# Kernel tuning notes

Measured on AMD Instinct MI355X. Metric: run time of the kernel, lower is better.

Reference implementation:

```python
import jax, jax.numpy as jnp
import numpy as np

STRIDES = (8, 16, 32, 64, 128)
NUM_CONVS = 4
GROUPS = 32
EPS = 1e-5
FEAT_SHAPES = [(8, 256, 100, 152), (8, 256, 50, 76), (8, 256, 25, 38), (8, 256, 13, 19), (8, 256, 7, 10)]


def _conv3x3(x, w, b):
    # x: [B,C,H,W], w: [O,I,3,3] -> SAME padding, stride 1
    y = jax.lax.conv_general_dilated(x, w, (1, 1), 'SAME', dimension_numbers=('NCHW', 'OIHW', 'NCHW'))
    return y + b[None, :, None, None]


def _group_norm(x, g, b):
    B, C, H, W = x.shape
    xr = x.reshape(B, GROUPS, C // GROUPS, H, W)
    m = xr.mean(axis=(2, 3, 4), keepdims=True)
    v = xr.var(axis=(2, 3, 4), keepdims=True)
    xr = (xr - m) * jax.lax.rsqrt(v + EPS)
    return xr.reshape(B, C, H, W) * g[None, :, None, None] + b[None, :, None, None]


def _head(feats, cls_w, cls_b, cls_gn_g, cls_gn_b, box_w, box_b, box_gn_g, box_gn_b,
          logits_w, logits_b, ctr_w, ctr_b, reg_w, reg_b, scales):
    outs = []
    for l, f in enumerate(feats):
        ct, bt = f, f
        for i in range(NUM_CONVS):  # fixed-depth tower loop
            ct = jax.nn.relu(_group_norm(_conv3x3(ct, cls_w[i], cls_b[i]), cls_gn_g[i], cls_gn_b[i]))
            bt = jax.nn.relu(_group_norm(_conv3x3(bt, box_w[i], box_b[i]), box_gn_g[i], box_gn_b[i]))
        logits = _conv3x3(ct, logits_w, logits_b)          # [B,80,H,W]
        ctr = _conv3x3(ct, ctr_w, ctr_b)                   # [B,1,H,W]
        reg = jnp.exp(scales[l] * _conv3x3(bt, reg_w, reg_b))  # [B,4,H,W], torch.exp(Scale(bbox_pred))
        B = f.shape[0]
        outs.append(jnp.concatenate([logits, reg, ctr], axis=1).reshape(B, -1))
    return jnp.concatenate(outs, axis=1)  # [B, sum_l 85*H_l*W_l]


def _locations(feats):
    # FCOS grid locations: (x,y) center of each stride cell, per level, concatenated
    locs = []
    for l, f in enumerate(feats):
        h, w = f.shape[-2:]
        s = STRIDES[l]
        sx = jnp.arange(w, dtype=jnp.float32) * s + s // 2
        sy = jnp.arange(h, dtype=jnp.float32) * s + s // 2
        yy, xx = jnp.meshgrid(sy, sx, indexing='ij')
        locs.append(jnp.stack([xx.reshape(-1), yy.reshape(-1)], axis=1))
    return jnp.concatenate(locs, axis=0)  # [sum HW, 2]


def setup_inputs() -> dict:
    key = jax.random.key(0)
    ks = jax.random.split(key, 12)
    d = {}
    for i, s in enumerate(FEAT_SHAPES):
        d['feat%d' % i] = jax.random.normal(ks[i], s, dtype=jnp.float32)

    def w(k, shape):
        return jax.random.normal(k, shape, dtype=jnp.float32) * 0.01  # init std=0.01

    d['cls_w'] = w(ks[5], (NUM_CONVS, 256, 256, 3, 3))
    d['cls_b'] = jnp.zeros((NUM_CONVS, 256), jnp.float32)
    d['cls_gn_g'] = jnp.ones((NUM_CONVS, 256), jnp.float32)
    d['cls_gn_b'] = jnp.zeros((NUM_CONVS, 256), jnp.float32)
    d['box_w'] = w(ks[6], (NUM_CONVS, 256, 256, 3, 3))
    d['box_b'] = jnp.zeros((NUM_CONVS, 256), jnp.float32)
    d['box_gn_g'] = jnp.ones((NUM_CONVS, 256), jnp.float32)
    d['box_gn_b'] = jnp.zeros((NUM_CONVS, 256), jnp.float32)
    d['logits_w'] = w(ks[7], (80, 256, 3, 3))
    d['logits_b'] = jnp.full((80,), -float(np.log((1.0 - 0.01) / 0.01)), jnp.float32)  # prior_prob bias
    d['ctr_w'] = w(ks[8], (1, 256, 3, 3))
    d['ctr_b'] = jnp.zeros((1,), jnp.float32)
    d['reg_w'] = w(ks[9], (4, 256, 3, 3))
    d['reg_b'] = jnp.zeros((4,), jnp.float32)
    d['scales'] = jnp.ones((5,), jnp.float32)
    return d


def reference(feat0, feat1, feat2, feat3, feat4, cls_w, cls_b, cls_gn_g, cls_gn_b,
              box_w, box_b, box_gn_g, box_gn_b, logits_w, logits_b, ctr_w, ctr_b,
              reg_w, reg_b, scales):
    feats = [feat0, feat1, feat2, feat3, feat4]
    out = _head(feats, cls_w, cls_b, cls_gn_g, cls_gn_b, box_w, box_b, box_gn_g, box_gn_b,
                logits_w, logits_b, ctr_w, ctr_b, reg_w, reg_b, scales)
    locs = _locations(feats)
    return out, locs
```

## Files before the change

### kernel.cpp

```cpp
#include <hip/hip_runtime.h>
#include <hip/hip_bf16.h>

#define TOT85 1722695ULL

using short8 = __attribute__((ext_vector_type(8))) short;
using f32x4  = __attribute__((ext_vector_type(4))) float;

struct Feat5 { const float* p[5]; };

__device__ __forceinline__ float bfbits2f(short u) {
  return __uint_as_float(((unsigned int)(unsigned short)u) << 16);
}
__device__ __forceinline__ short f2bfbits(float f) {
  __hip_bfloat16 h = __float2bfloat16(f);
  return *reinterpret_cast<short*>(&h);
}

#define LVL_TABLES                                                              \
  constexpr int kH[5] = {100, 50, 25, 13, 7};                                   \
  constexpr int kW[5] = {152, 76, 38, 19, 10};                                  \
  constexpr int kNTx[5] = {10, 5, 3, 2, 1};                                     \
  constexpr int kCumT[5] = {0, 130, 165, 177, 181};                             \
  constexpr int kCumHW[5] = {0, 15200, 19000, 19950, 20197};                    \
  constexpr float kInv[5] = {1.f / 121600.f, 1.f / 30400.f, 1.f / 7600.f,       \
                             1.f / 1976.f, 1.f / 560.f};

__global__ __launch_bounds__(256) void repack_k(const float* __restrict__ src,
                                                __hip_bfloat16* __restrict__ dst,
                                                int O, int NOCP, int ocoff) {
  int idx = blockIdx.x * 256 + threadIdx.x;
  if (idx >= O * 2304) return;
  int o = idx / 2304;
  int r = idx - o * 2304;
  int i = r / 9;
  int t = r - i * 9;
  dst[((size_t)(t * 8 + (i >> 5)) * NOCP + (o + ocoff)) * 32 + (i & 31)] =
      __float2bfloat16(src[idx]);
}

__global__ void locations_all_k(float* __restrict__ out) {
  LVL_TABLES
  constexpr int kStride[5] = {8, 16, 32, 64, 128};
  int i = blockIdx.x * 256 + threadIdx.x;
  if (i >= 20267) return;
  int lvl = (i >= 15200) + (i >= 19000) + (i >= 19950) + (i >= 20197);
  int local = i - kCumHW[lvl];
  int W = kW[lvl];
  float s = (float)kStride[lvl];
  int y = local / W, x = local - y * W;
  out[2 * i + 0] = x * s + 0.5f * s;
  out[2 * i + 1] = y * s + 0.5f * s;
}

template <bool NORM_IN, bool SRC_NCHW>
__global__ __launch_bounds__(256, 2) void conv_tower_k(
    Feat5 feats, const __hip_bfloat16* __restrict__ srcb_base,
    const __hip_bfloat16* __restrict__ wpk, const float* __restrict__ bias,
    const float* __restrict__ statsInBase, const float* __restrict__ gamma,
    const float* __restrict__ beta, __hip_bfloat16* __restrict__ dstBase,
    float* __restrict__ statsOutBase) {
  LVL_TABLES
  __shared__ __align__(16) short s_in[180 * 72];
  __shared__ float s_red[64];
  __shared__ float s_a[256], s_c[256];

  const int tid = threadIdx.x;
  const int lane = tid & 63;
  const int wave = tid >> 6;
  const int wm = wave >> 1;
  const int wn = wave & 1;
  const int bx = blockIdx.x;
  const int lvl = (bx >= 130) + (bx >= 165) + (bx >= 177) + (bx >= 181);
  const int H = kH[lvl], W = kW[lvl], nTx = kNTx[lvl];
  const int tloc = bx - kCumT[lvl];
  const int ty = tloc / nTx, tx = tloc - ty * nTx;
  const int x0 = tx * 16, y0 = ty * 8;
  const int b = blockIdx.z;
  const int HW = H * W;
  const size_t lbase = (size_t)2048 * kCumHW[lvl];
  const int l15 = lane & 15;
  const int kg = lane >> 4;
  const int q8x = (tid & 7) * 8;

  if (tid < 64) s_red[tid] = 0.f;
  if (NORM_IN) {
    const float* statsIn = statsInBase + (size_t)lvl * 4096;
    float inv_cnt = kInv[lvl];
    int g = tid >> 3;
    float s = statsIn[(b * 32 + g) * 2 + 0];
    float ss = statsIn[(b * 32 + g) * 2 + 1];
    float m = s * inv_cnt;
    float var = fmaf(-m, m, ss * inv_cnt);
    float rs = rsqrtf(var + 1e-5f);
    float avv = rs * gamma[tid];
    s_a[tid] = avv;
    s_c[tid] = fmaf(-m, avv, beta[tid]);
  }

  f32x4 acc[4][8];
#pragma unroll
  for (int m = 0; m < 4; ++m)
#pragma unroll
    for (int n = 0; n < 8; ++n) acc[m][n] = (f32x4){0.f, 0.f, 0.f, 0.f};

  const short* wlane = (const short*)wpk + ((wn * 128 + l15) * 32 + kg * 8);

  const int pixN = tid;
  int prowN = pixN / 18;
  int pcolN = pixN - prowN * 18;
  const int gyN = y0 + prowN - 1, gxN = x0 + pcolN - 1;
  const bool validN = (pixN < 180) && (gyN >= 0 && gyN < H && gxN >= 0 && gxN < W);

  for (int c = 0; c < 4; ++c) {
    const int ic0 = c * 64;

    short8 pv[6];
    float fv[32];
    if (SRC_NCHW) {
      const float* srcf = feats.p[lvl];
      if (validN) {
        const float* p = srcf + (((size_t)(b * 256 + ic0)) * H + gyN) * W + gxN;
#pragma unroll
        for (int j = 0; j < 32; ++j) fv[j] = p[(size_t)j * HW];
      }
    } else {
      const short* srcb = (const short*)srcb_base + lbase;
#pragma unroll
      for (int r = 0; r < 6; ++r) {
        int idx = r * 256 + tid;
        pv[r] = (short8)0;
        if (idx < 1440) {
          int px = idx >> 3;
          int prow = px / 18;
          int pcol = px - prow * 18;
          int gy = y0 + prow - 1, gx = x0 + pcol - 1;
          if (gy >= 0 && gy < H && gx >= 0 && gx < W)
            pv[r] = *(const short8*)(srcb +
                                     ((((size_t)b * H + gy) * W + gx) * 256 + ic0 + q8x));
        }
      }
    }

    __syncthreads();

    if (SRC_NCHW) {
      const float* srcf = feats.p[lvl];
      if (pixN < 180) {
        short8 sv[4];
        if (validN) {
#pragma unroll
          for (int q = 0; q < 4; ++q)
#pragma unroll
            for (int j = 0; j < 8; ++j) sv[q][j] = f2bfbits(fv[q * 8 + j]);
        } else {
#pragma unroll
          for (int q = 0; q < 4; ++q) sv[q] = (short8)0;
        }
#pragma unroll
        for (int q = 0; q < 4; ++q) *(short8*)(s_in + pixN * 72 + q * 8) = sv[q];
        if (validN) {
          const float* p = srcf + (((size_t)(b * 256 + ic0 + 32)) * H + gyN) * W + gxN;
#pragma unroll
          for (int j = 0; j < 32; ++j) fv[j] = p[(size_t)j * HW];
#pragma unroll
          for (int q = 0; q < 4; ++q)
#pragma unroll
            for (int j = 0; j < 8; ++j) sv[q][j] = f2bfbits(fv[q * 8 + j]);
        }
#pragma unroll
        for (int q = 0; q < 4; ++q) *(short8*)(s_in + pixN * 72 + 32 + q * 8) = sv[q];
      }
    } else {
      float av[8], cv[8];
#pragma unroll
      for (int j = 0; j < 8; ++j) {
        int c2 = ic0 + q8x + j;
        av[j] = s_a[c2];
        cv[j] = s_c[c2];
      }
#pragma unroll
      for (int r = 0; r < 6; ++r) {
        int idx = r * 256 + tid;
        if (idx < 1440) {
          int px = idx >> 3;
          int prow = px / 18;
          int pcol = px - prow * 18;
          int gy = y0 + prow - 1, gx = x0 + pcol - 1;
          short8 o8 = (short8)0;
          if (gy >= 0 && gy < H && gx >= 0 && gx < W) {
#pragma unroll
            for (int j = 0; j < 8; ++j)
              o8[j] = f2bfbits(fmaxf(fmaf(bfbits2f(pv[r][j]), av[j], cv[j]), 0.f));
          }
          *(short8*)(s_in + px * 72 + q8x) = o8;
        }
      }
    }
    __syncthreads();

    const short* wcb = wlane + (size_t)c * 2 * 8192;
    short8 bwA[8], bwB[8];
#pragma unroll
    for (int n = 0; n < 8; ++n) bwA[n] = *(const short8*)(wcb + n * 512);

    auto kbody = [&](int k, short8* curw, short8* nxtw) {
      if (k < 17) {
        int kn = k + 1;
        const short* wt = wcb + ((size_t)((kn >> 1) * 8 + (kn & 1))) * 8192;
#pragma unroll
        for (int n = 0; n < 8; ++n) nxtw[n] = *(const short8*)(wt + n * 512);
      }
      const int tap = k >> 1, sub = k & 1;
      const int dy = tap / 3, dx = tap - dy * 3;
      short8 af[4];
#pragma unroll
      for (int m = 0; m < 4; ++m)
        af[m] = *(const short8*)(s_in + ((wm * 4 + m + dy) * 18 + (l15 + dx)) * 72 +
                                 sub * 32 + kg * 8);
#pragma unroll
      for (int m = 0; m < 4; ++m)
#pragma unroll
        for (int n = 0; n < 8; ++n)
          acc[m][n] = __builtin_amdgcn_mfma_f32_16x16x32_bf16(af[m], curw[n], acc[m][n], 0, 0, 0);
    };
#pragma unroll
    for (int k = 0; k < 18; k += 2) {
      kbody(k, bwA, bwB);
      kbody(k + 1, bwB, bwA);
    }
  }

  short* dst = (short*)dstBase + lbase;
  const int masks[5] = {1, 2, 4, 16, 32};
#pragma unroll
  for (int n = 0; n < 8; ++n) {
    int oc_g = wn * 128 + n * 16 + l15;
    float bv = bias[oc_g];
    float lsum = 0.f, lssq = 0.f;
#pragma unroll
    for (int m = 0; m < 4; ++m) {
      int oy = y0 + wm * 4 + m;
#pragma unroll
      for (int r = 0; r < 4; ++r) {
        int ox = x0 + kg * 4 + r;
        bool valid = (oy < H) && (ox < W);
        float v = acc[m][n][r] + bv;
        if (valid) {
          dst[(((size_t)b * H + oy) * W + ox) * 256 + oc_g] = f2bfbits(v);
          lsum += v;
          lssq += v * v;
        }
      }
    }
#pragma unroll
    for (int s = 0; s < 5; ++s) {
      lsum += __shfl_xor(lsum, masks[s], 64);
      lssq += __shfl_xor(lssq, masks[s], 64);
    }
    if ((lane & 55) == 0) {
      int g2 = ((wn * 8 + n) * 2 + ((lane >> 3) & 1)) * 2;
      atomicAdd(&s_red[g2 + 0], lsum);
      atomicAdd(&s_red[g2 + 1], lssq);
    }
  }
  __syncthreads();
  float* statsOut = statsOutBase + (size_t)lvl * 4096;
  if (tid < 64) atomicAdd(&statsOut[(size_t)b * 64 + tid], s_red[tid]);
}

template <int NREP, int OUT_MODE>
__global__ __launch_bounds__(256, 3) void conv_head_k(
    const __hip_bfloat16* __restrict__ srcb_base, const __hip_bfloat16* __restrict__ wpk,
    const float* __restrict__ bias, const float* __restrict__ bias2,
    const float* __restrict__ statsInBase, const float* __restrict__ gamma,
    const float* __restrict__ beta, float* __restrict__ out,
    const float* __restrict__ scales, int NOCP) {
  LVL_TABLES
  __shared__ __align__(16) short s_in[180 * 40];
  __shared__ float s_a[256], s_c[256];

  const int tid = threadIdx.x;
  const int lane = tid & 63;
  const int wave = tid >> 6;
  const int wm = wave >> 1;
  const int wn = wave & 1;
  const int bx = blockIdx.x;
  const int lvl = (bx >= 130) + (bx >= 165) + (bx >= 177) + (bx >= 181);
  const int H = kH[lvl], W = kW[lvl], nTx = kNTx[lvl];
  const int tloc = bx - kCumT[lvl];
  const int ty = tloc / nTx, tx = tloc - ty * nTx;
  const int x0 = tx * 16, y0 = ty * 8;
  const int b = blockIdx.z;
  const int HW = H * W;
  const size_t lbase = (size_t)2048 * kCumHW[lvl];
  float* out_lvl = out + (size_t)85 * kCumHW[lvl];
  const int l15 = lane & 15;
  const int kg = lane >> 4;
  const int q8 = (tid & 3) * 8;

  {
    const float* statsIn = statsInBase + (size_t)lvl * 4096;
    float inv_cnt = kInv[lvl];
    int g = tid >> 3;
    float s = statsIn[(b * 32 + g) * 2 + 0];
    float ss = statsIn[(b * 32 + g) * 2 + 1];
    float m = s * inv_cnt;
    float var = fmaf(-m, m, ss * inv_cnt);
    float rs = rsqrtf(var + 1e-5f);
    float avv = rs * gamma[tid];
    s_a[tid] = avv;
    s_c[tid] = fmaf(-m, avv, beta[tid]);
  }

  f32x4 acc[4][NREP];
#pragma unroll
  for (int m = 0; m < 4; ++m)
#pragma unroll
    for (int n = 0; n < NREP; ++n) acc[m][n] = (f32x4){0.f, 0.f, 0.f, 0.f};

  const short* wlane = (const short*)wpk + ((wn * NREP * 16 + l15) * 32 + kg * 8);
  const size_t TAPSTR = (size_t)8 * NOCP * 32;

  for (int chunk = 0; chunk < 8; ++chunk) {
    const int ic0 = chunk * 32;
    __syncthreads();
    {
      const short* srcb = (const short*)srcb_base + lbase;
      float av[8], cv[8];
#pragma unroll
      for (int j = 0; j < 8; ++j) {
        int c2 = ic0 + q8 + j;
        av[j] = s_a[c2];
        cv[j] = s_c[c2];
      }
      for (int idx = tid; idx < 720; idx += 256) {
        int pix = idx >> 2;
        int prow = pix / 18;
        int pcol = pix - prow * 18;
        int gy = y0 + prow - 1, gx = x0 + pcol - 1;
        short8 o8 = (short8)0;
        if (gy >= 0 && gy < H && gx >= 0 && gx < W) {
          const short* sp = srcb + ((((size_t)b * H + gy) * W + gx) * 256 + ic0 + q8);
          short8 v8 = *(const short8*)sp;
#pragma unroll
          for (int j = 0; j < 8; ++j)
            o8[j] = f2bfbits(fmaxf(fmaf(bfbits2f(v8[j]), av[j], cv[j]), 0.f));
        }
        *(short8*)(s_in + pix * 40 + q8) = o8;
      }
    }
    __syncthreads();

    const short* wch = wlane + (size_t)chunk * NOCP * 32;
    short8 bwA[NREP], bwB[NREP];
#pragma unroll
    for (int n = 0; n < NREP; ++n) bwA[n] = *(const short8*)(wch + n * 512);

    auto tapbody = [&](int tap, short8* curw, short8* nxtw) {
      if (tap < 8) {
        const short* wt = wch + (size_t)(tap + 1) * TAPSTR;
#pragma unroll
        for (int n = 0; n < NREP; ++n) nxtw[n] = *(const short8*)(wt + n * 512);
      }
      const int dy = tap / 3, dx = tap - dy * 3;
      short8 af[4];
#pragma unroll
      for (int m = 0; m < 4; ++m)
        af[m] = *(const short8*)(s_in + ((wm * 4 + m + dy) * 18 + (l15 + dx)) * 40 + kg * 8);
#pragma unroll
      for (int m = 0; m < 4; ++m)
#pragma unroll
        for (int n = 0; n < NREP; ++n)
          acc[m][n] = __builtin_amdgcn_mfma_f32_16x16x32_bf16(af[m], curw[n], acc[m][n], 0, 0, 0);
    };
#pragma unroll
    for (int tap = 0; tap < 9; tap += 2) {
      tapbody(tap, bwA, bwB);
      if (tap + 1 < 9) tapbody(tap + 1, bwB, bwA);
    }
  }

#pragma unroll
  for (int n = 0; n < NREP; ++n) {
    int oc_l = wn * NREP * 16 + n * 16 + l15;
    int oc_valid = (OUT_MODE == 1) ? 81 : 4;
    float bv;
    if (OUT_MODE == 1)
      bv = (oc_l < 80) ? bias[oc_l] : ((oc_l == 80) ? bias2[0] : 0.f);
    else
      bv = (oc_l < oc_valid) ? bias[oc_l] : 0.f;
#pragma unroll
    for (int m = 0; m < 4; ++m) {
      int oy = y0 + wm * 4 + m;
#pragma unroll
      for (int r = 0; r < 4; ++r) {
        int ox = x0 + kg * 4 + r;
        bool valid = (oy < H) && (ox < W) && (oc_l < oc_valid);
        float v = acc[m][n][r] + bv;
        if (valid) {
          if (OUT_MODE == 1) {
            int och = (oc_l == 80) ? 84 : oc_l;
            out_lvl[(size_t)b * TOT85 + (size_t)och * HW + oy * W + ox] = v;
          } else {
            out_lvl[(size_t)b * TOT85 + (size_t)(80 + oc_l) * HW + oy * W + ox] =
                expf(scales[lvl] * v);
          }
        }
      }
    }
  }
}

extern "C" void kernel_launch(void* const* d_in, const int* in_sizes, int n_in,
                              void* d_out_v, int out_size, void* d_ws, size_t ws_size,
                              hipStream_t stream) {
  (void)in_sizes; (void)n_in; (void)out_size; (void)ws_size;

  Feat5 feats;
  for (int i = 0; i < 5; ++i) feats.p[i] = (const float*)d_in[i];
  Feat5 featsNull;
  for (int i = 0; i < 5; ++i) featsNull.p[i] = nullptr;
  const float* cls_w = (const float*)d_in[5];
  const float* cls_b = (const float*)d_in[6];
  const float* cls_g = (const float*)d_in[7];
  const float* cls_bb = (const float*)d_in[8];
  const float* box_w = (const float*)d_in[9];
  const float* box_b = (const float*)d_in[10];
  const float* box_g = (const float*)d_in[11];
  const float* box_bb = (const float*)d_in[12];
  const float* logits_w = (const float*)d_in[13];
  const float* logits_b = (const float*)d_in[14];
  const float* ctr_w = (const float*)d_in[15];
  const float* ctr_b = (const float*)d_in[16];
  const float* reg_w = (const float*)d_in[17];
  const float* reg_b = (const float*)d_in[18];
  const float* scales = (const float*)d_in[19];
  float* d_out = (float*)d_out_v;

  char* wsp = (char*)d_ws;
  size_t off = 0;
  auto carve = [&](size_t bytes) -> char* {
    char* p = wsp + off;
    off += (bytes + 255) & ~(size_t)255;
    return p;
  };
  const size_t ALLE = (size_t)8 * 20267 * 256;
  __hip_bfloat16* bufA = (__hip_bfloat16*)carve(ALLE * 2);
  __hip_bfloat16* bufB = (__hip_bfloat16*)carve(ALLE * 2);
  const size_t TW = (size_t)9 * 8 * 256 * 32;
  __hip_bfloat16* wpk_cls = (__hip_bfloat16*)carve(4 * TW * 2);
  __hip_bfloat16* wpk_box = (__hip_bfloat16*)carve(4 * TW * 2);
  __hip_bfloat16* wpk_clsh = (__hip_bfloat16*)carve((size_t)9 * 8 * 96 * 32 * 2);
  __hip_bfloat16* wpk_regh = (__hip_bfloat16*)carve((size_t)9 * 8 * 32 * 32 * 2);
  float* stats_all = (float*)carve((size_t)40 * 512 * 4);

  hipMemsetAsync(stats_all, 0, (size_t)40 * 512 * 4, stream);

  auto rp = [&](const float* s, __hip_bfloat16* d, int O, int NOCP, int ocoff) {
    int total = O * 2304;
    hipLaunchKernelGGL(repack_k, dim3((total + 255) / 256), dim3(256), 0, stream, s, d, O, NOCP,
                       ocoff);
  };
  for (int i = 0; i < 4; ++i) {
    rp(cls_w + (size_t)i * 256 * 2304, wpk_cls + (size_t)i * TW, 256, 256, 0);
    rp(box_w + (size_t)i * 256 * 2304, wpk_box + (size_t)i * TW, 256, 256, 0);
  }
  rp(logits_w, wpk_clsh, 80, 96, 0);
  rp(ctr_w, wpk_clsh, 1, 96, 80);
  rp(reg_w, wpk_regh, 4, 32, 0);

  const size_t OUT0 = (size_t)8 * TOT85;
  hipLaunchKernelGGL(locations_all_k, dim3(80), dim3(256), 0, stream, d_out + OUT0);

  dim3 grid(182, 1, 8);
  dim3 blk(256);

  for (int t = 0; t < 2; ++t) {
    const __hip_bfloat16* wpkT = (t == 0) ? wpk_cls : wpk_box;
    const float* bt = (t == 0) ? cls_b : box_b;
    const float* gt = (t == 0) ? cls_g : box_g;
    const float* bbt = (t == 0) ? cls_bb : box_bb;
    auto slot = [&](int i) { return stats_all + (size_t)(t * 4 + i) * 512; };

    hipLaunchKernelGGL((conv_tower_k<false, true>), grid, blk, 0, stream, feats,
                       (const __hip_bfloat16*)nullptr, wpkT, bt, (const float*)nullptr,
                       (const float*)nullptr, (const float*)nullptr, bufA, slot(0));
    __hip_bfloat16* cur = bufA;
    __hip_bfloat16* nxt = bufB;
    for (int i = 1; i < 4; ++i) {
      hipLaunchKernelGGL((conv_tower_k<true, false>), grid, blk, 0, stream, featsNull,
                         (const __hip_bfloat16*)cur, wpkT + (size_t)i * TW, bt + i * 256,
                         slot(i - 1), gt + (i - 1) * 256, bbt + (i - 1) * 256, nxt, slot(i));
      __hip_bfloat16* tmp = cur;
      cur = nxt;
      nxt = tmp;
    }
    if (t == 0) {
      hipLaunchKernelGGL((conv_head_k<3, 1>), grid, blk, 0, stream, (const __hip_bfloat16*)cur,
                         wpk_clsh, logits_b, ctr_b, slot(3), gt + 3 * 256, bbt + 3 * 256,
                         d_out, scales, 96);
    } else {
      hipLaunchKernelGGL((conv_head_k<1, 2>), grid, blk, 0, stream, (const __hip_bfloat16*)cur,
                         wpk_regh, reg_b, (const float*)nullptr, slot(3), gt + 3 * 256,
                         bbt + 3 * 256, d_out, scales, 32);
    }
  }
}
```

Measured before the change: 2.446 ms.

## Run cls and box tower convolutions in one launch per layer

Each tower conv kernel takes two pointer sets and picks one by blockIdx.y, so the cls and box towers run together in a single grid of twice the size. This halves the number of tower launches and doubles the blocks per launch, which helps fill the GPU on small levels and tail waves. The eight separate weight repack launches are also merged into one. The fused path needs twice the activation workspace and falls back to the sequential schedule when ws_size is too small.

```diff
diff --git a/kernel.cpp b/kernel.cpp
--- a/kernel.cpp
+++ b/kernel.cpp
@@ -7,6 +7,17 @@
 using f32x4  = __attribute__((ext_vector_type(4))) float;
 
 struct Feat5 { const float* p[5]; };
+struct TowerPtrs {
+  const __hip_bfloat16* wpk;
+  const float* bias;
+  const float* statsIn;
+  const float* gamma;
+  const float* beta;
+  const __hip_bfloat16* src;
+  __hip_bfloat16* dst;
+  float* statsOut;
+};
+struct TowerArgs { TowerPtrs t0, t1; };
 
 __device__ __forceinline__ float bfbits2f(short u) {
   return __uint_as_float(((unsigned int)(unsigned short)u) << 16);
@@ -24,6 +35,25 @@
   constexpr int kCumHW[5] = {0, 15200, 19000, 19950, 20197};                    \
   constexpr float kInv[5] = {1.f / 121600.f, 1.f / 30400.f, 1.f / 7600.f,       \
                              1.f / 1976.f, 1.f / 560.f};
+
+__global__ __launch_bounds__(256) void repack_tower_k(const float* __restrict__ cls_w,
+                                                      const float* __restrict__ box_w,
+                                                      __hip_bfloat16* __restrict__ dst_cls,
+                                                      __hip_bfloat16* __restrict__ dst_box) {
+  const size_t TW = (size_t)9 * 8 * 256 * 32;
+  int y = blockIdx.y;
+  const float* src = (y < 4) ? cls_w + (size_t)y * 256 * 2304
+                             : box_w + (size_t)(y - 4) * 256 * 2304;
+  __hip_bfloat16* dst = (y < 4) ? dst_cls + (size_t)y * TW
+                                : dst_box + (size_t)(y - 4) * TW;
+  int idx = blockIdx.x * 256 + threadIdx.x;
+  int o = idx / 2304;
+  int r = idx - o * 2304;
+  int i = r / 9;
+  int t = r - i * 9;
+  dst[((size_t)(t * 8 + (i >> 5)) * 256 + o) * 32 + (i & 31)] =
+      __float2bfloat16(src[idx]);
+}
 
 __global__ __launch_bounds__(256) void repack_k(const float* __restrict__ src,
                                                 __hip_bfloat16* __restrict__ dst,
@@ -53,16 +83,14 @@
 }
 
 template <bool NORM_IN, bool SRC_NCHW>
-__global__ __launch_bounds__(256, 2) void conv_tower_k(
-    Feat5 feats, const __hip_bfloat16* __restrict__ srcb_base,
-    const __hip_bfloat16* __restrict__ wpk, const float* __restrict__ bias,
-    const float* __restrict__ statsInBase, const float* __restrict__ gamma,
-    const float* __restrict__ beta, __hip_bfloat16* __restrict__ dstBase,
-    float* __restrict__ statsOutBase) {
+__global__ __launch_bounds__(256, 2) void conv_tower_k(Feat5 feats, TowerArgs args) {
   LVL_TABLES
   __shared__ __align__(16) short s_in[180 * 72];
   __shared__ float s_red[64];
   __shared__ float s_a[256], s_c[256];
+
+  TowerPtrs P;
+  if (blockIdx.y == 0) P = args.t0; else P = args.t1;
 
   const int tid = threadIdx.x;
   const int lane = tid & 63;
@@ -84,7 +112,7 @@
 
   if (tid < 64) s_red[tid] = 0.f;
   if (NORM_IN) {
-    const float* statsIn = statsInBase + (size_t)lvl * 4096;
+    const float* statsIn = P.statsIn + (size_t)lvl * 4096;
     float inv_cnt = kInv[lvl];
     int g = tid >> 3;
     float s = statsIn[(b * 32 + g) * 2 + 0];
@@ -92,9 +120,9 @@
     float m = s * inv_cnt;
     float var = fmaf(-m, m, ss * inv_cnt);
     float rs = rsqrtf(var + 1e-5f);
-    float avv = rs * gamma[tid];
+    float avv = rs * P.gamma[tid];
     s_a[tid] = avv;
-    s_c[tid] = fmaf(-m, avv, beta[tid]);
+    s_c[tid] = fmaf(-m, avv, P.beta[tid]);
   }
 
   f32x4 acc[4][8];
@@ -103,7 +131,7 @@
 #pragma unroll
     for (int n = 0; n < 8; ++n) acc[m][n] = (f32x4){0.f, 0.f, 0.f, 0.f};
 
-  const short* wlane = (const short*)wpk + ((wn * 128 + l15) * 32 + kg * 8);
+  const short* wlane = (const short*)P.wpk + ((wn * 128 + l15) * 32 + kg * 8);
 
   const int pixN = tid;
   int prowN = pixN / 18;
@@ -124,7 +152,7 @@
         for (int j = 0; j < 32; ++j) fv[j] = p[(size_t)j * HW];
       }
     } else {
-      const short* srcb = (const short*)srcb_base + lbase;
+      const short* srcb = (const short*)P.src + lbase;
 #pragma unroll
       for (int r = 0; r < 6; ++r) {
         int idx = r * 256 + tid;
@@ -230,12 +258,12 @@
     }
   }
 
-  short* dst = (short*)dstBase + lbase;
+  short* dst = (short*)P.dst + lbase;
   const int masks[5] = {1, 2, 4, 16, 32};
 #pragma unroll
   for (int n = 0; n < 8; ++n) {
     int oc_g = wn * 128 + n * 16 + l15;
-    float bv = bias[oc_g];
+    float bv = P.bias[oc_g];
     float lsum = 0.f, lssq = 0.f;
 #pragma unroll
     for (int m = 0; m < 4; ++m) {
@@ -264,7 +292,7 @@
     }
   }
   __syncthreads();
-  float* statsOut = statsOutBase + (size_t)lvl * 4096;
+  float* statsOut = P.statsOut + (size_t)lvl * 4096;
   if (tid < 64) atomicAdd(&statsOut[(size_t)b * 64 + tid], s_red[tid]);
 }
 
@@ -414,12 +442,10 @@
 extern "C" void kernel_launch(void* const* d_in, const int* in_sizes, int n_in,
                               void* d_out_v, int out_size, void* d_ws, size_t ws_size,
                               hipStream_t stream) {
-  (void)in_sizes; (void)n_in; (void)out_size; (void)ws_size;
+  (void)in_sizes; (void)n_in; (void)out_size;
 
   Feat5 feats;
   for (int i = 0; i < 5; ++i) feats.p[i] = (const float*)d_in[i];
-  Feat5 featsNull;
-  for (int i = 0; i < 5; ++i) featsNull.p[i] = nullptr;
   const float* cls_w = (const float*)d_in[5];
   const float* cls_b = (const float*)d_in[6];
   const float* cls_g = (const float*)d_in[7];
@@ -445,9 +471,22 @@
     return p;
   };
   const size_t ALLE = (size_t)8 * 20267 * 256;
-  __hip_bfloat16* bufA = (__hip_bfloat16*)carve(ALLE * 2);
-  __hip_bfloat16* bufB = (__hip_bfloat16*)carve(ALLE * 2);
+  const size_t ALLEb = ALLE * 2;
   const size_t TW = (size_t)9 * 8 * 256 * 32;
+  const size_t FIXED = 8 * TW * 2 + (size_t)9 * 8 * 96 * 32 * 2 +
+                       (size_t)9 * 8 * 32 * 32 * 2 + (size_t)40 * 512 * 4 + 64 * 256;
+  const bool fused = (ws_size >= 4 * ALLEb + FIXED);
+
+  __hip_bfloat16 *bufCA, *bufCB, *bufBA, *bufBB;
+  bufCA = (__hip_bfloat16*)carve(ALLEb);
+  bufCB = (__hip_bfloat16*)carve(ALLEb);
+  if (fused) {
+    bufBA = (__hip_bfloat16*)carve(ALLEb);
+    bufBB = (__hip_bfloat16*)carve(ALLEb);
+  } else {
+    bufBA = bufCA;
+    bufBB = bufCB;
+  }
   __hip_bfloat16* wpk_cls = (__hip_bfloat16*)carve(4 * TW * 2);
   __hip_bfloat16* wpk_box = (__hip_bfloat16*)carve(4 * TW * 2);
   __hip_bfloat16* wpk_clsh = (__hip_bfloat16*)carve((size_t)9 * 8 * 96 * 32 * 2);
@@ -456,15 +495,13 @@
 
   hipMemsetAsync(stats_all, 0, (size_t)40 * 512 * 4, stream);
 
+  hipLaunchKernelGGL(repack_tower_k, dim3(2304, 8), dim3(256), 0, stream, cls_w, box_w,
+                     wpk_cls, wpk_box);
   auto rp = [&](const float* s, __hip_bfloat16* d, int O, int NOCP, int ocoff) {
     int total = O * 2304;
     hipLaunchKernelGGL(repack_k, dim3((total + 255) / 256), dim3(256), 0, stream, s, d, O, NOCP,
                        ocoff);
   };
-  for (int i = 0; i < 4; ++i) {
-    rp(cls_w + (size_t)i * 256 * 2304, wpk_cls + (size_t)i * TW, 256, 256, 0);
-    rp(box_w + (size_t)i * 256 * 2304, wpk_box + (size_t)i * TW, 256, 256, 0);
-  }
   rp(logits_w, wpk_clsh, 80, 96, 0);
   rp(ctr_w, wpk_clsh, 1, 96, 80);
   rp(reg_w, wpk_regh, 4, 32, 0);
@@ -472,37 +509,72 @@
   const size_t OUT0 = (size_t)8 * TOT85;
   hipLaunchKernelGGL(locations_all_k, dim3(80), dim3(256), 0, stream, d_out + OUT0);
 
-  dim3 grid(182, 1, 8);
+  auto slot = [&](int t, int i) { return stats_all + (size_t)(t * 4 + i) * 512; };
+  auto mkPtrs = [&](int t, int i, const __hip_bfloat16* src, __hip_bfloat16* dst) {
+    TowerPtrs p;
+    p.wpk = ((t == 0) ? wpk_cls : wpk_box) + (size_t)i * TW;
+    p.bias = ((t == 0) ? cls_b : box_b) + i * 256;
+    p.statsIn = (i == 0) ? nullptr : slot(t, i - 1);
+    p.gamma = (i == 0) ? nullptr : ((t == 0) ? cls_g : box_g) + (i - 1) * 256;
+    p.beta = (i == 0) ? nullptr : ((t == 0) ? cls_bb : box_bb) + (i - 1) * 256;
+    p.src = src;
+    p.dst = dst;
+    p.statsOut = slot(t, i);
+    return p;
+  };
+
   dim3 blk(256);
-
-  for (int t = 0; t < 2; ++t) {
-    const __hip_bfloat16* wpkT = (t == 0) ? wpk_cls : wpk_box;
-    const float* bt = (t == 0) ? cls_b : box_b;
-    const float* gt = (t == 0) ? cls_g : box_g;
-    const float* bbt = (t == 0) ? cls_bb : box_bb;
-    auto slot = [&](int i) { return stats_all + (size_t)(t * 4 + i) * 512; };
-
-    hipLaunchKernelGGL((conv_tower_k<false, true>), grid, blk, 0, stream, feats,
-                       (const __hip_bfloat16*)nullptr, wpkT, bt, (const float*)nullptr,
-                       (const float*)nullptr, (const float*)nullptr, bufA, slot(0));
-    __hip_bfloat16* cur = bufA;
-    __hip_bfloat16* nxt = bufB;
-    for (int i = 1; i < 4; ++i) {
-      hipLaunchKernelGGL((conv_tower_k<true, false>), grid, blk, 0, stream, featsNull,
-                         (const __hip_bfloat16*)cur, wpkT + (size_t)i * TW, bt + i * 256,
-                         slot(i - 1), gt + (i - 1) * 256, bbt + (i - 1) * 256, nxt, slot(i));
-      __hip_bfloat16* tmp = cur;
-      cur = nxt;
-      nxt = tmp;
-    }
-    if (t == 0) {
-      hipLaunchKernelGGL((conv_head_k<3, 1>), grid, blk, 0, stream, (const __hip_bfloat16*)cur,
-                         wpk_clsh, logits_b, ctr_b, slot(3), gt + 3 * 256, bbt + 3 * 256,
-                         d_out, scales, 96);
-    } else {
-      hipLaunchKernelGGL((conv_head_k<1, 2>), grid, blk, 0, stream, (const __hip_bfloat16*)cur,
-                         wpk_regh, reg_b, (const float*)nullptr, slot(3), gt + 3 * 256,
-                         bbt + 3 * 256, d_out, scales, 32);
-    }
-  }
-}
+  __hip_bfloat16 *curC = bufCA, *nxtC = bufCB, *curB = bufBA, *nxtB = bufBB;
+
+  if (fused) {
+    dim3 gridF(182, 2, 8);
+    for (int i = 0; i < 4; ++i) {
+      TowerArgs a;
+      if (i == 0) {
+        a.t0 = mkPtrs(0, 0, nullptr, curC);
+        a.t1 = mkPtrs(1, 0, nullptr, curB);
+        hipLaunchKernelGGL((conv_tower_k<false, true>), gridF, blk, 0, stream, feats, a);
+      } else {
+        a.t0 = mkPtrs(0, i, curC, nxtC);
+        a.t1 = mkPtrs(1, i, curB, nxtB);
+        hipLaunchKernelGGL((conv_tower_k<true, false>), gridF, blk, 0, stream, feats, a);
+        __hip_bfloat16* tc = curC; curC = nxtC; nxtC = tc;
+        __hip_bfloat16* tb = curB; curB = nxtB; nxtB = tb;
+      }
+    }
+    hipLaunchKernelGGL((conv_head_k<3, 1>), dim3(182, 1, 8), blk, 0, stream,
+                       (const __hip_bfloat16*)curC, wpk_clsh, logits_b, ctr_b, slot(0, 3),
+                       cls_g + 3 * 256, cls_bb + 3 * 256, d_out, scales, 96);
+    hipLaunchKernelGGL((conv_head_k<1, 2>), dim3(182, 1, 8), blk, 0, stream,
+                       (const __hip_bfloat16*)curB, wpk_regh, reg_b, (const float*)nullptr,
+                       slot(1, 3), box_g + 3 * 256, box_bb + 3 * 256, d_out, scales, 32);
+  } else {
+    dim3 gridS(182, 1, 8);
+    for (int t = 0; t < 2; ++t) {
+      __hip_bfloat16* cur = bufCA;
+      __hip_bfloat16* nxt = bufCB;
+      {
+        TowerArgs a;
+        a.t0 = mkPtrs(t, 0, nullptr, cur);
+        a.t1 = a.t0;
+        hipLaunchKernelGGL((conv_tower_k<false, true>), gridS, blk, 0, stream, feats, a);
+      }
+      for (int i = 1; i < 4; ++i) {
+        TowerArgs a;
+        a.t0 = mkPtrs(t, i, cur, nxt);
+        a.t1 = a.t0;
+        hipLaunchKernelGGL((conv_tower_k<true, false>), gridS, blk, 0, stream, feats, a);
+        __hip_bfloat16* tmp = cur; cur = nxt; nxt = tmp;
+      }
+      if (t == 0) {
+        hipLaunchKernelGGL((conv_head_k<3, 1>), gridS, blk, 0, stream,
+                           (const __hip_bfloat16*)cur, wpk_clsh, logits_b, ctr_b, slot(0, 3),
+                           cls_g + 3 * 256, cls_bb + 3 * 256, d_out, scales, 96);
+      } else {
+        hipLaunchKernelGGL((conv_head_k<1, 2>), gridS, blk, 0, stream,
+                           (const __hip_bfloat16*)cur, wpk_regh, reg_b, (const float*)nullptr,
+                           slot(1, 3), box_g + 3 * 256, box_bb + 3 * 256, d_out, scales, 32);
+      }
+    }
+  }
+}
```

After: 2.394 ms, median of 2. -2.2%, faster.
